# Kernel tuning notes

Hardware: AMD Instinct MI355X
Metric: run time of the kernel (lower is better)

Reference implementation:

```python
import jax, jax.numpy as jnp
import numpy as np

NUM_HEAD = 16

def _make_rope(max_len, dim_head, theta=10000.0):
    inv_freq = 1.0 / (theta ** (np.arange(0, dim_head, 2, dtype=np.float32) / dim_head))
    t = np.arange(max_len, dtype=np.float32)
    freqs = np.outer(t, inv_freq)  # [S, dim_head/2]
    return jnp.asarray(np.cos(freqs)), jnp.asarray(np.sin(freqs))

def setup_inputs() -> dict:
    key = jax.random.key(0)
    k1, k2, k3 = jax.random.split(key, 3)
    B, S, D = 2, 2048, 1024
    num_layer = 12
    std = 0.02 / np.sqrt(2 * num_layer)
    x = jax.random.normal(k1, (B, S, D), dtype=jnp.float32)
    wQKV = jax.random.normal(k2, (3 * D, D), dtype=jnp.float32) * std
    wOut = jax.random.normal(k3, (D, D), dtype=jnp.float32) * 0.02
    cos, sin = _make_rope(S, D // NUM_HEAD)
    return {"x": x, "wQKV": wQKV, "wOut": wOut, "cos": cos, "sin": sin}

def _apply_rope(t, cos, sin):
    # t: [B, H, S, dh]; cos/sin: [S, dh/2] -> broadcast [1,1,S,dh/2]
    te, to = t[..., ::2], t[..., 1::2]
    re = te * cos - to * sin
    ro = to * cos + te * sin
    return jnp.stack([re, ro], axis=-1).reshape(t.shape)

def reference(x, wQKV, wOut, cos, sin):
    B, S, D = x.shape
    H = NUM_HEAD
    dh = D // H
    qkv = x @ wQKV.T  # [B, S, 3D]
    q, k, v = jnp.split(qkv, 3, axis=-1)
    q = q.reshape(B, S, H, dh).transpose(0, 2, 1, 3)  # [B,H,S,dh]
    k = k.reshape(B, S, H, dh).transpose(0, 2, 1, 3)
    v = v.reshape(B, S, H, dh).transpose(0, 2, 1, 3)
    c = cos[:S][None, None]
    s = sin[:S][None, None]
    q = _apply_rope(q, c, s)
    k = _apply_rope(k, c, s)
    scores = jnp.einsum('bhsd,bhtd->bhst', q, k) / jnp.sqrt(jnp.asarray(dh, x.dtype))
    causal = jnp.tril(jnp.ones((S, S), dtype=bool))
    scores = jnp.where(causal, scores, jnp.asarray(-jnp.inf, scores.dtype))
    w = jax.nn.softmax(scores, axis=-1)
    out = jnp.einsum('bhst,bhtd->bhsd', w, v)  # [B,H,S,dh]
    out = out.transpose(0, 2, 1, 3).reshape(B, S, D)
    return out @ wOut.T
```

## Files before the change

kernel.cpp:

```cpp
#include <hip/hip_runtime.h>
#include <hip/hip_bf16.h>

typedef __attribute__((ext_vector_type(8))) short bf16x8;
typedef __attribute__((ext_vector_type(4))) short s16x4;
typedef __attribute__((ext_vector_type(4))) float f32x4;

__device__ __forceinline__ short f2bf(float f) {
    unsigned int u = __builtin_bit_cast(unsigned int, f);
    u += 0x7fffu + ((u >> 16) & 1u);
    return (short)(u >> 16);
}

#define GLDS(g, l) __builtin_amdgcn_global_load_lds( \
    (__attribute__((address_space(1))) void*)(g),    \
    (__attribute__((address_space(3))) void*)(l), 16, 0, 0)

#define BARSB() { __builtin_amdgcn_s_barrier(); __builtin_amdgcn_sched_barrier(0); }
#define VMC8()  { asm volatile("s_waitcnt vmcnt(8)" ::: "memory"); __builtin_amdgcn_sched_barrier(0); }
#define VMC7()  { asm volatile("s_waitcnt vmcnt(7)" ::: "memory"); __builtin_amdgcn_sched_barrier(0); }
#define VMC0()  { asm volatile("s_waitcnt vmcnt(0)" ::: "memory"); __builtin_amdgcn_sched_barrier(0); }

__global__ __launch_bounds__(256) void cvt_kernel(const float* __restrict__ in,
                                                  short* __restrict__ out, int n4) {
    int i = blockIdx.x * 256 + threadIdx.x;
    if (i >= n4) return;
    float4 v = reinterpret_cast<const float4*>(in)[i];
    s16x4 r = { f2bf(v.x), f2bf(v.y), f2bf(v.z), f2bf(v.w) };
    reinterpret_cast<s16x4*>(out)[i] = r;
}

#define LDP 72

__device__ __forceinline__ void load_a(const short* __restrict__ A, int wr, int lo, int hi,
                                       int mh, bf16x8 aF[4][2]) {
#pragma unroll
    for (int mi = 0; mi < 4; ++mi)
#pragma unroll
        for (int kk = 0; kk < 2; ++kk)
            aF[mi][kk] = *reinterpret_cast<const bf16x8*>(
                &A[(wr * 128 + mh * 64 + mi * 16 + lo) * 64 + (((kk * 4 + hi) ^ (lo & 7)) << 3)]);
}
__device__ __forceinline__ void load_b3(const short* __restrict__ B, int wc, int lo, int hi,
                                        bf16x8 bF[3][2]) {
#pragma unroll
    for (int ni = 0; ni < 3; ++ni)
#pragma unroll
        for (int kk = 0; kk < 2; ++kk)
            bF[ni][kk] = *reinterpret_cast<const bf16x8*>(
                &B[(wc * 48 + ni * 16 + lo) * 64 + (((kk * 4 + hi) ^ (lo & 7)) << 3)]);
}
__device__ __forceinline__ void mfma24(const bf16x8 aF[4][2], const bf16x8 bF[3][2],
                                       f32x4 acc[8][3], int mh) {
#pragma unroll
    for (int mi = 0; mi < 4; ++mi)
#pragma unroll
        for (int ni = 0; ni < 3; ++ni)
#pragma unroll
            for (int kk = 0; kk < 2; ++kk)
                acc[mh * 4 + mi][ni] = __builtin_amdgcn_mfma_f32_16x16x32_bf16(
                    aF[mi][kk], bF[ni][kk], acc[mh * 4 + mi][ni], 0, 0, 0);
}

__global__ __launch_bounds__(512, 1) void gemm_qkv_rope(
    const short* __restrict__ X, const short* __restrict__ W,
    const float* __restrict__ cosT, const float* __restrict__ sinT,
    short* __restrict__ Qo, short* __restrict__ Ko, short* __restrict__ Vo) {
    __shared__ short ldsA[2][16384];
    __shared__ short ldsB[2][12288];
    const int tid = threadIdx.x;
    const int lane = tid & 63;
    const int w = tid >> 6;
    const int lo = lane & 15, hi = lane >> 4;
    const int wr = w >> 2, wc = w & 3;
    const int lin = blockIdx.x;
    const int xcd = lin & 7;
    const int i_ = lin >> 3;
    const int m0 = ((xcd >> 1) * 4 + (i_ & 3)) * 256;
    const int n0 = ((xcd & 1) * 8 + (i_ >> 2)) * 192;

    f32x4 acc[8][3];
#pragma unroll
    for (int i = 0; i < 8; i++)
#pragma unroll
        for (int j = 0; j < 3; j++) acc[i][j] = {0.f, 0.f, 0.f, 0.f};

    const int srow8 = w * 8 + (lane >> 3);
    const int scx = (((lane & 7) ^ ((lane >> 3) & 7)) << 3);

#define STAGE_A(BUF, KT, IT) GLDS(X + (size_t)(m0 + (IT) * 64 + srow8) * 1024 + ((KT) << 6) + scx, \
                                  (char*)&ldsA[BUF][0] + (IT) * 8192 + w * 1024)
#define STAGE_B(BUF, KT, IT) GLDS(W + (size_t)(n0 + (IT) * 64 + srow8) * 1024 + ((KT) << 6) + scx, \
                                  (char*)&ldsB[BUF][0] + (IT) * 8192 + w * 1024)

    bf16x8 aF[4][2], bF[3][2];

    STAGE_B(0, 0, 0); STAGE_B(0, 0, 1); STAGE_B(0, 0, 2);
    STAGE_A(0, 0, 0); STAGE_A(0, 0, 1); STAGE_A(0, 0, 2); STAGE_A(0, 0, 3);

    for (int t = 0; t < 16; ++t) {
        const int c = t & 1;
        if (t < 15) {
            const int nb_ = c ^ 1, t1 = t + 1;
            STAGE_B(nb_, t1, 0); STAGE_B(nb_, t1, 1); STAGE_B(nb_, t1, 2);
            STAGE_A(nb_, t1, 0); STAGE_A(nb_, t1, 1); STAGE_A(nb_, t1, 2); STAGE_A(nb_, t1, 3);
            VMC7();
        } else {
            VMC0();
        }
        BARSB();
        load_a(&ldsA[c][0], wr, lo, hi, 0, aF);
        load_b3(&ldsB[c][0], wc, lo, hi, bF);
        mfma24(aF, bF, acc, 0);
        load_a(&ldsA[c][0], wr, lo, hi, 1, aF);
        mfma24(aF, bF, acc, 1);
        if (t < 15) BARSB();
    }
#undef STAGE_A
#undef STAGE_B

#pragma unroll
    for (int mi = 0; mi < 8; mi++) {
#pragma unroll
        for (int r = 0; r < 4; r++) {
            const int m = m0 + wr * 128 + mi * 16 + (hi << 2) + r;
            const int b_ = m >> 11;
            const int s_ = m & 2047;
#pragma unroll
            for (int ni = 0; ni < 3; ni++) {
                float v = acc[mi][ni][r];
                const int n = n0 + wc * 48 + ni * 16 + lo;
                const int region = n >> 10;
                const int c = n & 1023;
                const int h = c >> 6;
                const int d = c & 63;
                const size_t oidx = ((size_t)(b_ * 16 + h) * 2048 + s_) * 64 + d;
                if (region == 2) {
                    Vo[oidx] = f2bf(v);
                } else {
                    float other = __shfl_xor(v, 1, 64);
                    const int i2 = d >> 1;
                    float cs = cosT[s_ * 32 + i2];
                    float sn = sinT[s_ * 32 + i2];
                    float outv = (d & 1) ? (v * cs + other * sn) : (v * cs - other * sn);
                    if (region == 0) {
                        Qo[oidx] = f2bf(outv * 0.18033688f);
                    } else {
                        Ko[oidx] = f2bf(outv);
                    }
                }
            }
        }
    }
}

__device__ __forceinline__ void attn_tile_compute(
    const bf16x8 q0, const bf16x8 q1,
    const short* __restrict__ Ks,
    const short (*Vts)[LDP], short* __restrict__ Pw,
    const int lane, const int w, const bool diag,
    float& m_r, float& l_r, f32x4* __restrict__ o_acc) {
    const int lo = lane & 15, hi = lane >> 4;
    const int sx = lo & 7;

    f32x4 sc[4];
#pragma unroll
    for (int nb = 0; nb < 4; nb++) sc[nb] = {0.f, 0.f, 0.f, 0.f};
#pragma unroll
    for (int nb = 0; nb < 4; nb++) {
        const short* kr = &Ks[(nb * 16 + lo) * 64];
        bf16x8 k0 = *reinterpret_cast<const bf16x8*>(&kr[(hi ^ sx) << 3]);
        sc[nb] = __builtin_amdgcn_mfma_f32_16x16x32_bf16(k0, q0, sc[nb], 0, 0, 0);
        bf16x8 k1 = *reinterpret_cast<const bf16x8*>(&kr[((4 + hi) ^ sx) << 3]);
        sc[nb] = __builtin_amdgcn_mfma_f32_16x16x32_bf16(k1, q1, sc[nb], 0, 0, 0);
    }
    if (diag) {
        const int q_ = w * 16 + lo;
        const int kb = (hi << 2);
#pragma unroll
        for (int nb = 0; nb < 4; nb++) {
            const int k_ = nb * 16 + kb;
#pragma unroll
            for (int r = 0; r < 4; r++)
                if (k_ + r > q_) sc[nb][r] = -1e30f;
        }
    }

    float mx = sc[0][0];
#pragma unroll
    for (int nb = 0; nb < 4; nb++)
#pragma unroll
        for (int r = 0; r < 4; r++) mx = fmaxf(mx, sc[nb][r]);
    mx = fmaxf(mx, __shfl_xor(mx, 16, 64));
    mx = fmaxf(mx, __shfl_xor(mx, 32, 64));

    if (!__all(mx <= m_r + 8.0f)) {
        const float mnew = fmaxf(m_r, mx);
        const float alpha = __builtin_amdgcn_exp2f(m_r - mnew);
        m_r = mnew;
        l_r *= alpha;
        float aq[4];
#pragma unroll
        for (int r = 0; r < 4; r++) aq[r] = __shfl(alpha, (hi << 2) + r, 64);
#pragma unroll
        for (int db = 0; db < 4; db++)
#pragma unroll
            for (int r = 0; r < 4; r++) o_acc[db][r] *= aq[r];
    }

    float rs = 0.f;
#pragma unroll
    for (int nb = 0; nb < 4; nb++)
#pragma unroll
        for (int r = 0; r < 4; r++) {
            float e = __builtin_amdgcn_exp2f(sc[nb][r] - m_r);
            sc[nb][r] = e;
            rs += e;
        }
    rs += __shfl_xor(rs, 16, 64);
    rs += __shfl_xor(rs, 32, 64);
    l_r += rs;

    unsigned int* Pw32 = reinterpret_cast<unsigned int*>(Pw);
#pragma unroll
    for (int nb = 0; nb < 4; nb++)
#pragma unroll
        for (int rr = 0; rr < 2; rr++) {
            unsigned int pk;
            asm("v_cvt_pk_bf16_f32 %0, %1, %2"
                : "=v"(pk) : "v"(sc[nb][2 * rr]), "v"(sc[nb][2 * rr + 1]));
            Pw32[lo * (LDP / 2) + nb * 8 + (hi << 1) + rr] = pk;
        }

#pragma unroll
    for (int kk = 0; kk < 2; kk++) {
        bf16x8 pa = *reinterpret_cast<const bf16x8*>(&Pw[lo * LDP + kk * 32 + hi * 8]);
#pragma unroll
        for (int db = 0; db < 4; db++) {
            const int d = db * 16 + lo;
            const int tsw = (kk * 32 + hi * 8) ^ ((((d >> 3) & 7)) << 3);
            bf16x8 vb = *reinterpret_cast<const bf16x8*>(&Vts[d][tsw]);
            o_acc[db] = __builtin_amdgcn_mfma_f32_16x16x32_bf16(pa, vb, o_acc[db], 0, 0, 0);
        }
    }
}

__global__ __launch_bounds__(256) void attn_kernel(
    const short* __restrict__ Q, const short* __restrict__ K,
    const short* __restrict__ V, short* __restrict__ O) {
    __shared__ short Ks[2][64 * 64];
    __shared__ short Vts[2][64][LDP];
    __shared__ short Ps[4][16 * LDP];

    const int tid = threadIdx.x;
    const int lane = tid & 63;
    const int w = tid >> 6;
    const int lo = lane & 15, hi = lane >> 4;
    const int sx = lo & 7;
    const int lin = blockIdx.x;
    const int bh = lin & 31;
    const int qt = 31 - (lin >> 5);
    const int b_ = bh >> 4, h = bh & 15;
    const size_t base = (size_t)bh * 2048 * 64;

    const int krow = tid >> 2;
    const int cq = (tid & 3) * 2;
    const int ksw = krow & 7;

    bf16x8 q0, q1;
    {
        const short* src = Q + base + (size_t)(qt * 64 + krow) * 64 + cq * 8;
        bf16x8 a = *reinterpret_cast<const bf16x8*>(src);
        bf16x8 b = *reinterpret_cast<const bf16x8*>(src + 8);
        *reinterpret_cast<bf16x8*>(&Ks[0][krow * 64 + ((cq ^ ksw) << 3)]) = a;
        *reinterpret_cast<bf16x8*>(&Ks[0][krow * 64 + (((cq + 1) ^ ksw) << 3)]) = b;
        __syncthreads();
        q0 = *reinterpret_cast<const bf16x8*>(&Ks[0][(w * 16 + lo) * 64 + ((hi ^ sx) << 3)]);
        q1 = *reinterpret_cast<const bf16x8*>(&Ks[0][(w * 16 + lo) * 64 + (((4 + hi) ^ sx) << 3)]);
        __syncthreads();
    }

    float m_r = -1e30f, l_r = 0.f;
    f32x4 o_acc[4];
#pragma unroll
    for (int db = 0; db < 4; db++) o_acc[db] = {0.f, 0.f, 0.f, 0.f};

    const int u2 = tid >> 3;
    const int vdb8 = (tid & 7) * 8;
    const int vswz = (tid & 7) << 3;
    const int tw = (2 * u2) ^ vswz;

    bf16x8 kr0, kr1, vr0, vr1;
    kr0 = *reinterpret_cast<const bf16x8*>(K + base + (size_t)krow * 64 + cq * 8);
    kr1 = *reinterpret_cast<const bf16x8*>(K + base + (size_t)krow * 64 + cq * 8 + 8);
    vr0 = *reinterpret_cast<const bf16x8*>(V + base + (size_t)(2 * u2) * 64 + vdb8);
    vr1 = *reinterpret_cast<const bf16x8*>(V + base + (size_t)(2 * u2 + 1) * 64 + vdb8);

    int c = 0;
    for (int j = 0; j <= qt; j++) {
        *reinterpret_cast<bf16x8*>(&Ks[c][krow * 64 + ((cq ^ ksw) << 3)]) = kr0;
        *reinterpret_cast<bf16x8*>(&Ks[c][krow * 64 + (((cq + 1) ^ ksw) << 3)]) = kr1;
#pragma unroll
        for (int i = 0; i < 8; i++) {
            unsigned int pv = (unsigned int)(unsigned short)vr0[i] |
                              ((unsigned int)(unsigned short)vr1[i] << 16);
            *reinterpret_cast<unsigned int*>(&Vts[c][vdb8 + i][tw]) = pv;
        }
        __syncthreads();
        if (j < qt) {
            const size_t jb2 = (size_t)(j + 1) * 64;
            kr0 = *reinterpret_cast<const bf16x8*>(K + base + (jb2 + krow) * 64 + cq * 8);
            kr1 = *reinterpret_cast<const bf16x8*>(K + base + (jb2 + krow) * 64 + cq * 8 + 8);
            vr0 = *reinterpret_cast<const bf16x8*>(V + base + (jb2 + 2 * u2) * 64 + vdb8);
            vr1 = *reinterpret_cast<const bf16x8*>(V + base + (jb2 + 2 * u2 + 1) * 64 + vdb8);
        }

        attn_tile_compute(q0, q1, Ks[c], Vts[c], &Ps[w][0], lane, w, j == qt, m_r, l_r, o_acc);
        c ^= 1;
    }

    float inv[4];
#pragma unroll
    for (int r = 0; r < 4; r++) inv[r] = 1.f / __shfl(l_r, (hi << 2) + r, 64);

    short* Op = O + ((size_t)b_ * 2048) * 1024 + (size_t)h * 64;
#pragma unroll
    for (int r = 0; r < 4; r++) {
        const int row = qt * 64 + w * 16 + (hi << 2) + r;
#pragma unroll
        for (int db = 0; db < 4; db++)
            Op[(size_t)row * 1024 + db * 16 + lo] = f2bf(o_acc[db][r] * inv[r]);
    }
}

__global__ __launch_bounds__(256) void gemm_out(
    const short* __restrict__ A, const short* __restrict__ W,
    float* __restrict__ C) {
    __shared__ short As[2][128 * 64];
    __shared__ short Bs[2][128 * 64];
    const int tid = threadIdx.x;
    const int lane = tid & 63;
    const int w = tid >> 6;
    const int lo = lane & 15, hi = lane >> 4;
    const int wr = w >> 1, wc = w & 1;
    const int lin = blockIdx.x;
    const int wg = (lin & 7) * 32 + (lin >> 3);
    const int n0 = (wg & 7) * 128;
    const int m0 = (wg >> 3) * 128;
    const int K = 1024;

    f32x4 acc[4][4];
#pragma unroll
    for (int i = 0; i < 4; i++)
#pragma unroll
        for (int j = 0; j < 4; j++) acc[i][j] = {0.f, 0.f, 0.f, 0.f};

    const int srow = w * 8 + (lane >> 3);
    const int sc8 = (lane & 7) * 8;
    const short* gA = A + (size_t)(m0 + srow) * K + sc8;
    const short* gB = W + (size_t)(n0 + srow) * K + sc8;

#pragma unroll
    for (int it = 0; it < 4; it++)
        GLDS(gA + (size_t)it * 32 * K, (char*)As[0] + it * 4096 + w * 1024);
#pragma unroll
    for (int it = 0; it < 4; it++)
        GLDS(gB + (size_t)it * 32 * K, (char*)Bs[0] + it * 4096 + w * 1024);

    for (int t = 0; t < 16; t++) {
        const int c = t & 1;
        if (t < 15) {
            const int k1 = (t + 1) * 64;
#pragma unroll
            for (int it = 0; it < 4; it++)
                GLDS(gA + k1 + (size_t)it * 32 * K, (char*)As[c ^ 1] + it * 4096 + w * 1024);
#pragma unroll
            for (int it = 0; it < 4; it++)
                GLDS(gB + k1 + (size_t)it * 32 * K, (char*)Bs[c ^ 1] + it * 4096 + w * 1024);
            VMC8();
        } else {
            VMC0();
        }
        BARSB();
#pragma unroll
        for (int kk = 0; kk < 2; kk++) {
            bf16x8 a[4], b[4];
#pragma unroll
            for (int mi = 0; mi < 4; mi++)
                a[mi] = *reinterpret_cast<const bf16x8*>(
                    &As[c][(wr * 64 + mi * 16 + lo) * 64 + kk * 32 + hi * 8]);
#pragma unroll
            for (int ni = 0; ni < 4; ni++)
                b[ni] = *reinterpret_cast<const bf16x8*>(
                    &Bs[c][(wc * 64 + ni * 16 + lo) * 64 + kk * 32 + hi * 8]);
#pragma unroll
            for (int mi = 0; mi < 4; mi++)
#pragma unroll
                for (int ni = 0; ni < 4; ni++)
                    acc[mi][ni] = __builtin_amdgcn_mfma_f32_16x16x32_bf16(
                        a[mi], b[ni], acc[mi][ni], 0, 0, 0);
        }
        if (t < 15) BARSB();
    }

#pragma unroll
    for (int mi = 0; mi < 4; mi++) {
#pragma unroll
        for (int r = 0; r < 4; r++) {
            const int m = m0 + wr * 64 + mi * 16 + (hi << 2) + r;
#pragma unroll
            for (int ni = 0; ni < 4; ni++) {
                const int n = n0 + wc * 64 + ni * 16 + lo;
                C[(size_t)m * 1024 + n] = acc[mi][ni][r];
            }
        }
    }
}

extern "C" void kernel_launch(void* const* d_in, const int* in_sizes, int n_in,
                              void* d_out, int out_size, void* d_ws, size_t ws_size,
                              hipStream_t stream) {
    const float* x = (const float*)d_in[0];
    const float* wQKV = (const float*)d_in[1];
    const float* wOut = (const float*)d_in[2];
    const float* cosT = (const float*)d_in[3];
    const float* sinT = (const float*)d_in[4];
    float* out = (float*)d_out;

    char* ws = (char*)d_ws;
    const size_t MB = 1024 * 1024;
    short* xb    = (short*)(ws);
    short* wqkvb = (short*)(ws + 8 * MB);
    short* woutb = (short*)(ws + 14 * MB);
    short* Qbuf  = (short*)(ws + 16 * MB);
    short* Kbuf  = (short*)(ws + 24 * MB);
    short* Vbuf  = (short*)(ws + 32 * MB);
    short* Obuf  = (short*)(ws + 40 * MB);

    cvt_kernel<<<4096, 256, 0, stream>>>(x, xb, 1048576);
    cvt_kernel<<<3072, 256, 0, stream>>>(wQKV, wqkvb, 786432);
    cvt_kernel<<<1024, 256, 0, stream>>>(wOut, woutb, 262144);

    gemm_qkv_rope<<<256, 512, 0, stream>>>(xb, wqkvb, cosT, sinT, Qbuf, Kbuf, Vbuf);
    attn_kernel<<<1024, 256, 0, stream>>>(Qbuf, Kbuf, Vbuf, Obuf);
    gemm_out<<<256, 256, 0, stream>>>(Obuf, woutb, out);
}
```

Before: 124.2 us.

## Fuse conversion launches, pre-interleave RoPE tables, swizzle out-GEMM LDS layout

Merges the three fp32-to-bf16 conversion launches into one kernel, which also writes a transposed, interleaved cos/sin table. The QKV GEMM epilogue then reads that table with vectorized loads and walks rows in an order that reuses per-column index math. Separately, the output GEMM applies an XOR swizzle to its LDS layout to reduce bank conflicts. The intent is to cut launch overhead, epilogue load cost and LDS conflicts, in exchange for an extra table write and more workspace.

```diff
diff --git a/kernel.cpp b/kernel.cpp
--- a/kernel.cpp
+++ b/kernel.cpp
@@ -20,10 +20,27 @@
 #define VMC7()  { asm volatile("s_waitcnt vmcnt(7)" ::: "memory"); __builtin_amdgcn_sched_barrier(0); }
 #define VMC0()  { asm volatile("s_waitcnt vmcnt(0)" ::: "memory"); __builtin_amdgcn_sched_barrier(0); }
 
-__global__ __launch_bounds__(256) void cvt_kernel(const float* __restrict__ in,
-                                                  short* __restrict__ out, int n4) {
-    int i = blockIdx.x * 256 + threadIdx.x;
-    if (i >= n4) return;
+__global__ __launch_bounds__(256) void cvt_fused(const float* __restrict__ x,
+                                                 const float* __restrict__ wq,
+                                                 const float* __restrict__ wo,
+                                                 const float* __restrict__ cosT,
+                                                 const float* __restrict__ sinT,
+                                                 short* __restrict__ xb,
+                                                 short* __restrict__ wqb,
+                                                 short* __restrict__ wob,
+                                                 float2* __restrict__ csT) {
+    const int b = blockIdx.x;
+    if (b >= 8192) {
+        const int idx = (b - 8192) * 256 + threadIdx.x;
+        const int i2 = idx >> 11;
+        const int s = idx & 2047;
+        csT[idx] = make_float2(cosT[s * 32 + i2], sinT[s * 32 + i2]);
+        return;
+    }
+    const float* in; short* out; int i;
+    if (b < 4096)      { in = x;  out = xb;  i = b * 256 + threadIdx.x; }
+    else if (b < 7168) { in = wq; out = wqb; i = (b - 4096) * 256 + threadIdx.x; }
+    else               { in = wo; out = wob; i = (b - 7168) * 256 + threadIdx.x; }
     float4 v = reinterpret_cast<const float4*>(in)[i];
     s16x4 r = { f2bf(v.x), f2bf(v.y), f2bf(v.z), f2bf(v.w) };
     reinterpret_cast<s16x4*>(out)[i] = r;
@@ -63,7 +80,7 @@
 
 __global__ __launch_bounds__(512, 1) void gemm_qkv_rope(
     const short* __restrict__ X, const short* __restrict__ W,
-    const float* __restrict__ cosT, const float* __restrict__ sinT,
+    const float2* __restrict__ csT,
     short* __restrict__ Qo, short* __restrict__ Ko, short* __restrict__ Vo) {
     __shared__ short ldsA[2][16384];
     __shared__ short ldsB[2][12288];
@@ -118,35 +135,40 @@
 #undef STAGE_A
 #undef STAGE_B
 
-#pragma unroll
-    for (int mi = 0; mi < 8; mi++) {
-#pragma unroll
-        for (int r = 0; r < 4; r++) {
-            const int m = m0 + wr * 128 + mi * 16 + (hi << 2) + r;
-            const int b_ = m >> 11;
-            const int s_ = m & 2047;
-#pragma unroll
-            for (int ni = 0; ni < 3; ni++) {
-                float v = acc[mi][ni][r];
-                const int n = n0 + wc * 48 + ni * 16 + lo;
-                const int region = n >> 10;
-                const int c = n & 1023;
-                const int h = c >> 6;
-                const int d = c & 63;
-                const size_t oidx = ((size_t)(b_ * 16 + h) * 2048 + s_) * 64 + d;
-                if (region == 2) {
-                    Vo[oidx] = f2bf(v);
-                } else {
+    const int sfull = m0 + wr * 128 + (hi << 2);
+    const int b_ = sfull >> 11;
+    const int srow_ = sfull & 2047;
+#pragma unroll
+    for (int ni = 0; ni < 3; ni++) {
+        const int n = n0 + wc * 48 + ni * 16 + lo;
+        const int region = n >> 10;
+        const int c = n & 1023;
+        const int h = c >> 6;
+        const int d = c & 63;
+        const size_t obase = ((size_t)(b_ * 16 + h) * 2048 + srow_) * 64 + d;
+        if (region == 2) {
+#pragma unroll
+            for (int mi = 0; mi < 8; mi++)
+#pragma unroll
+                for (int r = 0; r < 4; r++)
+                    Vo[obase + (size_t)(mi * 16 + r) * 64] = f2bf(acc[mi][ni][r]);
+        } else {
+            short* dst = (region == 0) ? Qo : Ko;
+            const float scale = (region == 0) ? 0.18033688f : 1.0f;
+            const float2* csrow = csT + (size_t)(d >> 1) * 2048 + srow_;
+#pragma unroll
+            for (int mi = 0; mi < 8; mi++) {
+                float4 t0 = *reinterpret_cast<const float4*>(csrow + mi * 16);
+                float4 t1 = *reinterpret_cast<const float4*>(csrow + mi * 16 + 2);
+                const float cs_[4] = {t0.x, t0.z, t1.x, t1.z};
+                const float sn_[4] = {t0.y, t0.w, t1.y, t1.w};
+#pragma unroll
+                for (int r = 0; r < 4; r++) {
+                    float v = acc[mi][ni][r];
                     float other = __shfl_xor(v, 1, 64);
-                    const int i2 = d >> 1;
-                    float cs = cosT[s_ * 32 + i2];
-                    float sn = sinT[s_ * 32 + i2];
-                    float outv = (d & 1) ? (v * cs + other * sn) : (v * cs - other * sn);
-                    if (region == 0) {
-                        Qo[oidx] = f2bf(outv * 0.18033688f);
-                    } else {
-                        Ko[oidx] = f2bf(outv);
-                    }
+                    float outv = (d & 1) ? (v * cs_[r] + other * sn_[r])
+                                         : (v * cs_[r] - other * sn_[r]);
+                    dst[obase + (size_t)(mi * 16 + r) * 64] = f2bf(outv * scale);
                 }
             }
         }
@@ -355,9 +377,9 @@
         for (int j = 0; j < 4; j++) acc[i][j] = {0.f, 0.f, 0.f, 0.f};
 
     const int srow = w * 8 + (lane >> 3);
-    const int sc8 = (lane & 7) * 8;
-    const short* gA = A + (size_t)(m0 + srow) * K + sc8;
-    const short* gB = W + (size_t)(n0 + srow) * K + sc8;
+    const int scx = (((lane & 7) ^ ((lane >> 3) & 7)) << 3);
+    const short* gA = A + (size_t)(m0 + srow) * K + scx;
+    const short* gB = W + (size_t)(n0 + srow) * K + scx;
 
 #pragma unroll
     for (int it = 0; it < 4; it++)
@@ -387,11 +409,11 @@
 #pragma unroll
             for (int mi = 0; mi < 4; mi++)
                 a[mi] = *reinterpret_cast<const bf16x8*>(
-                    &As[c][(wr * 64 + mi * 16 + lo) * 64 + kk * 32 + hi * 8]);
+                    &As[c][(wr * 64 + mi * 16 + lo) * 64 + (((kk * 4 + hi) ^ (lo & 7)) << 3)]);
 #pragma unroll
             for (int ni = 0; ni < 4; ni++)
                 b[ni] = *reinterpret_cast<const bf16x8*>(
-                    &Bs[c][(wc * 64 + ni * 16 + lo) * 64 + kk * 32 + hi * 8]);
+                    &Bs[c][(wc * 64 + ni * 16 + lo) * 64 + (((kk * 4 + hi) ^ (lo & 7)) << 3)]);
 #pragma unroll
             for (int mi = 0; mi < 4; mi++)
 #pragma unroll
@@ -435,12 +457,10 @@
     short* Kbuf  = (short*)(ws + 24 * MB);
     short* Vbuf  = (short*)(ws + 32 * MB);
     short* Obuf  = (short*)(ws + 40 * MB);
-
-    cvt_kernel<<<4096, 256, 0, stream>>>(x, xb, 1048576);
-    cvt_kernel<<<3072, 256, 0, stream>>>(wQKV, wqkvb, 786432);
-    cvt_kernel<<<1024, 256, 0, stream>>>(wOut, woutb, 262144);
-
-    gemm_qkv_rope<<<256, 512, 0, stream>>>(xb, wqkvb, cosT, sinT, Qbuf, Kbuf, Vbuf);
+    float2* csT  = (float2*)(ws + 48 * MB);
+
+    cvt_fused<<<8448, 256, 0, stream>>>(x, wQKV, wOut, cosT, sinT, xb, wqkvb, woutb, csT);
+    gemm_qkv_rope<<<256, 512, 0, stream>>>(xb, wqkvb, csT, Qbuf, Kbuf, Vbuf);
     attn_kernel<<<1024, 256, 0, stream>>>(Qbuf, Kbuf, Vbuf, Obuf);
     gemm_out<<<256, 256, 0, stream>>>(Obuf, woutb, out);
 }
```

After: 108.2 us, median of 3. 1.15x faster.
